# Optimization experiments

Hardware: AMD Instinct MI355X
Metric: run time of the kernel (lower is better)

## Reference

```python
import jax, jax.numpy as jnp
import numpy as np

B, D, N, H = 2, 512, 2048, 8
DK = D // H
EPS = 1e-5


def conv1x1(x, w, b):
    # kernel-size-1 Conv1d == channel-mixing GEMM: (o,i) x (b,i,n) -> (b,o,n)
    return jnp.einsum('oi,bin->bon', w, x) + b[None, :, None]


def setup_inputs() -> dict:
    key = jax.random.key(0)
    ks = jax.random.split(key, 20)
    s = 0.02
    return {
        'init_query': jax.random.normal(ks[0], (B, D, N), jnp.float32),
        'key_t': jax.random.normal(ks[1], (B, D, N), jnp.float32),
        'value': jax.random.normal(ks[2], (B, D, N), jnp.float32),
        'mask': jax.random.randint(ks[3], (B, 1, N, N), 0, 2, jnp.int32),
        'Wq': jax.random.normal(ks[4], (D, D), jnp.float32) * s,
        'bq': jax.random.normal(ks[5], (D,), jnp.float32) * s,
        'Wk': jax.random.normal(ks[6], (D, D), jnp.float32) * s,
        'bk': jax.random.normal(ks[7], (D,), jnp.float32) * s,
        'Wv': jax.random.normal(ks[8], (D, D), jnp.float32) * s,
        'bv': jax.random.normal(ks[9], (D,), jnp.float32) * s,
        'Wm': jax.random.normal(ks[10], (D, D), jnp.float32) * s,
        'bm': jax.random.normal(ks[11], (D,), jnp.float32) * s,
        'W1': jax.random.normal(ks[12], (2 * D, 2 * D), jnp.float32) * s,
        'b1': jax.random.normal(ks[13], (2 * D,), jnp.float32) * s,
        'gamma': jnp.ones((2 * D,), jnp.float32),
        'beta': jnp.zeros((2 * D,), jnp.float32),
        'rmean': jax.random.normal(ks[14], (2 * D,), jnp.float32) * s,
        'rvar': jnp.abs(jax.random.normal(ks[15], (2 * D,), jnp.float32)) * 0.1 + 0.5,
        'W2': jax.random.normal(ks[16], (D, 2 * D), jnp.float32) * s,
        'b2': jnp.zeros((D,), jnp.float32),  # nn.init.constant_(bias, 0.0)
    }


def reference(init_query, key_t, value, mask, Wq, bq, Wk, bk, Wv, bv, Wm, bm,
              W1, b1, gamma, beta, rmean, rvar, W2, b2):
    # projections, split channels into (d_k, n_heads) exactly like torch .view
    q = conv1x1(init_query, Wq, bq).reshape(B, DK, H, N)
    k = conv1x1(key_t, Wk, bk).reshape(B, DK, H, N)
    v = conv1x1(value, Wv, bv).reshape(B, DK, H, N)
    scores = jnp.einsum('bdhn,bdhm->bhnm', q, k) / jnp.sqrt(jnp.float32(DK))
    scores = jnp.where(mask == 0, jnp.float32(-1e9), scores)
    attn = jax.nn.softmax(scores, axis=-1)
    x = jnp.einsum('bhnm,bdhm->bdhn', attn, v).reshape(B, D, N)
    x = conv1x1(x, Wm, bm)
    x = jnp.concatenate([x, init_query], axis=1)  # (B, 2D, N)
    h = conv1x1(x, W1, b1)
    # BatchNorm1d (inference mode with running stats) + ReLU
    h = (h - rmean[None, :, None]) * (gamma / jnp.sqrt(rvar + EPS))[None, :, None] + beta[None, :, None]
    h = jax.nn.relu(h)
    return conv1x1(h, W2, b2)
```

## Files before the change

### kernel.cpp

```cpp
#include <hip/hip_runtime.h>

typedef unsigned short u16;
typedef unsigned int u32;
typedef unsigned long long u64;
typedef long long i64;
typedef __bf16 bf16x8 __attribute__((ext_vector_type(8)));
typedef u16 u16x8 __attribute__((ext_vector_type(8)));
typedef u32 u32x2 __attribute__((ext_vector_type(2)));
typedef float f32x4 __attribute__((ext_vector_type(4)));

#define DEV __device__ __forceinline__

constexpr int BB = 2, DD = 512, NN = 2048, HH = 8, DKc = 64, D2 = 1024;

constexpr float QSC = 0.125f * 1.44269504088896340736f;

constexpr i64 OFF_CAT = 0;
constexpr i64 OFF_XKT = 8388608;
constexpr i64 OFF_XVT = 12582912;
constexpr i64 OFF_QH  = 16777216;
constexpr i64 OFF_KH  = 20971520;
constexpr i64 OFF_VT  = 25165824;
constexpr i64 OFF_OT  = 29360128;
constexpr i64 OFF_HT  = 33554432;
constexpr i64 OFF_WQP = 41943040;
constexpr i64 OFF_WKP = 42467328;
constexpr i64 OFF_WVP = 42991616;
constexpr i64 OFF_WMP = 43515904;
constexpr i64 OFF_W1B = 44040192;
constexpr i64 OFF_W2B = 46137344;
constexpr i64 OFF_BQP = 47185920;
constexpr i64 OFF_BKP = 47187968;
constexpr i64 OFF_BVP = 47190016;
constexpr i64 OFF_BNA = 47192064;
constexpr i64 OFF_BNC = 47196160;
constexpr i64 OFF_MSK = 47200256;

DEV u16 f2bf(float f) {
  u32 u = __float_as_uint(f);
  u = u + 0x7FFFu + ((u >> 16) & 1u);
  return (u16)(u >> 16);
}

DEV u32 packbf(float lo, float hi) {
  return __builtin_amdgcn_perm(__float_as_uint(hi), __float_as_uint(lo), 0x07060302u);
}

DEV float fexp2(float x) {
#if __has_builtin(__builtin_amdgcn_exp2f)
  return __builtin_amdgcn_exp2f(x);
#else
  return exp2f(x);
#endif
}

DEV bf16x8 ldfrag(const u16* p) {
  bf16x8 v;
  __builtin_memcpy(&v, __builtin_assume_aligned(p, 16), 16);
  return v;
}

DEV bf16x8 ldfrag8(const u16* p) {
  bf16x8 v;
  __builtin_memcpy(&v, __builtin_assume_aligned(p, 8), 16);
  return v;
}

DEV bf16x8 ones8() {
  u16x8 u = {0x3F80, 0x3F80, 0x3F80, 0x3F80, 0x3F80, 0x3F80, 0x3F80, 0x3F80};
  bf16x8 v;
  __builtin_memcpy(&v, &u, 16);
  return v;
}

DEV void gload16(const void* g, void* lds) {
  __builtin_amdgcn_global_load_lds((__attribute__((address_space(1))) void*)g,
                                   (__attribute__((address_space(3))) void*)lds, 16, 0, 0);
}

DEV f32x4 mfma16(bf16x8 a, bf16x8 b, f32x4 c) {
  return __builtin_amdgcn_mfma_f32_16x16x32_bf16(a, b, c, 0, 0, 0);
}

__global__ __launch_bounds__(256) void prep_kernel(
    const float* __restrict__ Wq, const float* __restrict__ Wk, const float* __restrict__ Wv,
    const float* __restrict__ Wm, const float* __restrict__ W1, const float* __restrict__ W2,
    const float* __restrict__ bq, const float* __restrict__ bk, const float* __restrict__ bv,
    const float* __restrict__ b1, const float* __restrict__ gamma_, const float* __restrict__ beta_,
    const float* __restrict__ rmean, const float* __restrict__ rvar, const int* __restrict__ mask,
    u16* __restrict__ wqp, u16* __restrict__ wkp, u16* __restrict__ wvp, u16* __restrict__ wmp,
    u16* __restrict__ w1b, u16* __restrict__ w2b,
    float* __restrict__ bqp, float* __restrict__ bkp, float* __restrict__ bvp,
    float* __restrict__ bna, float* __restrict__ bnc, u32* __restrict__ mw) {
  const int blk = blockIdx.x, t = threadIdx.x;
  if (blk < 768) {
    const int which = blk >> 8, lb = blk & 255;
    const float* W = which == 0 ? Wq : (which == 1 ? Wk : Wv);
    u16* dst = which == 0 ? wqp : (which == 1 ? wkp : wvp);
    for (int e = lb * 256 + t; e < 262144; e += 65536) {
      int op = e >> 9, i = e & 511;
      int dk = op & 63, h = op >> 6;
      dst[e] = f2bf(W[(dk * 8 + h) * 512 + i]);
    }
  } else if (blk < 1024) {
    const int lb = blk - 768;
    for (int e = lb * 256 + t; e < 262144; e += 65536) {
      int o = e >> 9, c = e & 511;
      int dk = c & 63, h = c >> 6;
      wmp[e] = f2bf(Wm[o * 512 + dk * 8 + h]);
    }
  } else if (blk < 1536) {
    const int lb = blk - 1024;
    for (int e = lb * 256 + t; e < 1048576; e += 131072) w1b[e] = f2bf(W1[e]);
  } else if (blk < 1792) {
    const int lb = blk - 1536;
    for (int e = lb * 256 + t; e < 524288; e += 65536) w2b[e] = f2bf(W2[e]);
  } else if (blk == 1792) {
    for (int e = t; e < 512; e += 256) {
      int src = (e & 63) * 8 + (e >> 6);
      bqp[e] = bq[src]; bkp[e] = bk[src]; bvp[e] = bv[src];
    }
    for (int e = t; e < 1024; e += 256) {
      float a = gamma_[e] * rsqrtf(rvar[e] + 1e-5f);
      bna[e] = a;
      bnc[e] = (b1[e] - rmean[e]) * a + beta_[e];
    }
  } else {
    const int tid = (blk - 1793) * 256 + t;
    const i64 base = (i64)tid * 32;
    const int4* mp = (const int4*)(mask + base);
    u32 word = 0;
#pragma unroll
    for (int j = 0; j < 8; ++j) {
      int4 x = mp[j];
      u32 nib = (x.x != 0 ? 1u : 0u) | (x.y != 0 ? 2u : 0u) | (x.z != 0 ? 4u : 0u) |
                (x.w != 0 ? 8u : 0u);
      word |= nib << (j * 4);
    }
    mw[tid] = word;
  }
}

__global__ __launch_bounds__(256) void transpose_cvt(const float* __restrict__ iq,
                                                     const float* __restrict__ kt,
                                                     const float* __restrict__ vv,
                                                     u16* __restrict__ cat, u16* __restrict__ xkt,
                                                     u16* __restrict__ xvt) {
  __shared__ float tile[32][33];
  const int z = blockIdx.z, tensor = z >> 1, b = z & 1;
  const float* src = tensor == 0 ? iq : (tensor == 1 ? kt : vv);
  src += (i64)b * DD * NN;
  u16* dst; i64 ldd; int coff;
  if (tensor == 0)      { dst = cat + (i64)b * NN * D2; ldd = D2; coff = DD; }
  else if (tensor == 1) { dst = xkt + (i64)b * NN * DD; ldd = DD; coff = 0; }
  else                  { dst = xvt + (i64)b * NN * DD; ldd = DD; coff = 0; }
  const int x0 = blockIdx.x * 32, y0 = blockIdx.y * 32;
  const int col = threadIdx.x & 31, rg = threadIdx.x >> 5;
#pragma unroll
  for (int i = 0; i < 4; ++i) {
    int row = rg + i * 8;
    tile[row][col] = src[(i64)(y0 + row) * NN + x0 + col];
  }
  __syncthreads();
#pragma unroll
  for (int i = 0; i < 4; ++i) {
    int rr = rg + i * 8;
    dst[(i64)(x0 + rr) * ldd + coff + y0 + col] = f2bf(tile[col][rr]);
  }
}

template <int AM, int AN>
DEV void gemm_core(const u16* __restrict__ A, i64 lda, const u16* __restrict__ Bp, i64 ldb,
                   int K, u16* As, u16* Bs, f32x4 (&acc)[AM][AN]) {
  constexpr int BM = AM * 32, BN = AN * 32;
  const int t = threadIdx.x, w = t >> 6, l = t & 63, quad = l >> 4, l15 = l & 15;
  const int wm = (w >> 1) * AM * 16, wn = (w & 1) * AN * 16;
  for (int kk = 0; kk < K; kk += 64) {
    __syncthreads();
#pragma unroll
    for (int j = 0; j < BM / 32; ++j) {
      int ch = j * 256 + w * 64 + l, r = ch >> 3, c = ch & 7;
      gload16(A + (i64)r * lda + kk + ((c ^ (r & 7)) << 3), As + (j * 256 + w * 64) * 8);
    }
#pragma unroll
    for (int j = 0; j < BN / 32; ++j) {
      int ch = j * 256 + w * 64 + l, r = ch >> 3, c = ch & 7;
      gload16(Bp + (i64)r * ldb + kk + ((c ^ (r & 7)) << 3), Bs + (j * 256 + w * 64) * 8);
    }
    __syncthreads();
#pragma unroll
    for (int kc = 0; kc < 2; ++kc) {
      const int sw = ((kc * 4 + quad) ^ (l15 & 7)) << 3;
      bf16x8 af[AM], bfr[AN];
#pragma unroll
      for (int i = 0; i < AM; ++i) af[i] = ldfrag(&As[(wm + i * 16 + l15) * 64 + sw]);
#pragma unroll
      for (int j = 0; j < AN; ++j) bfr[j] = ldfrag(&Bs[(wn + j * 16 + l15) * 64 + sw]);
#pragma unroll
      for (int i = 0; i < AM; ++i)
#pragma unroll
        for (int j = 0; j < AN; ++j) acc[i][j] = mfma16(af[i], bfr[j], acc[i][j]);
    }
  }
}

__global__ __launch_bounds__(256) void qkv_gemm(const u16* __restrict__ cat,
                                                const u16* __restrict__ xkt,
                                                const u16* __restrict__ xvt,
                                                const u16* __restrict__ wqp,
                                                const u16* __restrict__ wkp,
                                                const u16* __restrict__ wvp,
                                                const float* __restrict__ bqp,
                                                const float* __restrict__ bkp,
                                                const float* __restrict__ bvp,
                                                u16* __restrict__ qh, u16* __restrict__ kh,
                                                u16* __restrict__ vt) {
  __shared__ __align__(16) u16 As[128 * 64];
  __shared__ __align__(16) u16 Bs[64 * 64];
  const int z = blockIdx.z, op = z >> 1, b = z & 1;
  const int t = threadIdx.x, w = t >> 6, l = t & 63, quad = l >> 4, l15 = l & 15;
  const int wm = (w >> 1) * 64, wn = (w & 1) * 32;
  int mx, ny;
  const u16 *A, *Bp;
  i64 lda, ldb;
  if (op < 2) {
    mx = blockIdx.x; ny = blockIdx.y;
    A = (op == 0 ? cat + DD : xkt);
    lda = (op == 0 ? D2 : DD);
    A += (i64)b * NN * lda + (i64)mx * 128 * lda;
    Bp = (op == 0 ? wqp : wkp) + (i64)ny * 64 * DD;
    ldb = DD;
  } else {
    int f = blockIdx.x * 8 + blockIdx.y;
    mx = f >> 5; ny = f & 31;
    A = wvp + (i64)mx * 128 * DD; lda = DD;
    Bp = xvt + (i64)b * NN * DD + (i64)ny * 64 * DD; ldb = DD;
  }
  f32x4 acc[4][2] = {};
  gemm_core<4, 2>(A, lda, Bp, ldb, DD, As, Bs, acc);

  const int rowBase = mx * 128 + wm + quad * 4;
  const int colBase = ny * 64 + wn + l15;
  if (op < 2) {
    const float* bias = (op == 0 ? bqp : bkp);
    const float sc = (op == 0 ? QSC : 1.f);
    u16* dst = (op == 0 ? qh : kh) + (i64)b * HH * NN * DKc;
#pragma unroll
    for (int j = 0; j < 2; ++j) {
      const int col = colBase + j * 16;
      const float cA = bias[col];
#pragma unroll
      for (int i = 0; i < 4; ++i)
#pragma unroll
        for (int r = 0; r < 4; ++r) {
          const int row = rowBase + i * 16 + r;
          dst[(i64)(col >> 6) * (NN * 64) + (i64)row * 64 + (col & 63)] =
              f2bf((acc[i][j][r] + cA) * sc);
        }
    }
  } else {
    u16* dst = vt + (i64)b * HH * DKc * NN;
#pragma unroll
    for (int j = 0; j < 2; ++j) {
      const int col = colBase + j * 16;
      const int colp = (col & ~63) | (((col & 15) << 2) | ((col >> 4) & 3));
#pragma unroll
      for (int i = 0; i < 4; ++i)
#pragma unroll
        for (int r = 0; r < 4; ++r) {
          const int row = rowBase + i * 16 + r;
          dst[(i64)row * NN + colp] = f2bf(acc[i][j][r] + bvp[row]);
        }
    }
  }
}

struct GArgs {
  const u16* A; i64 lda, sAb;
  const u16* B; i64 ldb, sBb;
  void* C; i64 ldc, sCb;
  const float* p1; const float* p2;
  int K;
};

template <int MODE, int AM, int AN>
__global__ __launch_bounds__(256) void gemm_bt(GArgs g) {
  __shared__ __align__(16) u16 As[AM * 32 * 64];
  __shared__ __align__(16) u16 Bs[AN * 32 * 64];
  const int t = threadIdx.x, w = t >> 6, l = t & 63, quad = l >> 4, l15 = l & 15;
  const int wm = (w >> 1) * AM * 16, wn = (w & 1) * AN * 16;
  const int bz = blockIdx.z;
  const u16* A = g.A + (i64)bz * g.sAb + (i64)blockIdx.x * (AM * 32) * g.lda;
  const u16* Bp = g.B + (i64)bz * g.sBb + (i64)blockIdx.y * (AN * 32) * g.ldb;
  f32x4 acc[AM][AN] = {};
  gemm_core<AM, AN>(A, g.lda, Bp, g.ldb, g.K, As, Bs, acc);

  const int rowBase = blockIdx.x * (AM * 32) + wm + quad * 4;
  const int colBase = blockIdx.y * (AN * 32) + wn + l15;
#pragma unroll
  for (int j = 0; j < AN; ++j) {
    const int col = colBase + j * 16;
    float cA = 0.f, cB = 0.f;
    if (MODE == 0) cA = g.p1[col];
    if (MODE == 3) { cA = g.p1[col]; cB = g.p2[col]; }
#pragma unroll
    for (int i = 0; i < AM; ++i) {
#pragma unroll
      for (int r = 0; r < 4; ++r) {
        const int row = rowBase + i * 16 + r;
        float v = acc[i][j][r];
        if (MODE == 0) {
          ((u16*)g.C + (i64)bz * g.sCb)[(i64)row * g.ldc + col] = f2bf(v + cA);
        } else if (MODE == 3) {
          float x = v * cA + cB;
          ((u16*)g.C + (i64)bz * g.sCb)[(i64)row * g.ldc + col] = f2bf(x > 0.f ? x : 0.f);
        } else {
          ((float*)g.C + (i64)bz * g.sCb)[(i64)row * g.ldc + col] = v + g.p1[row];
        }
      }
    }
  }
}

__global__ __launch_bounds__(256) void flash_attn(const u16* __restrict__ Qh,
                                                  const u16* __restrict__ Kh,
                                                  const u16* __restrict__ Vt,
                                                  const u64* __restrict__ MW,
                                                  u16* __restrict__ Ot) {
  __shared__ __align__(16) u16 Qs[64 * 64];
  __shared__ __align__(16) u16 Ks[64 * 64];
  __shared__ __align__(16) u16 Vs[64 * 64];
  __shared__ __align__(16) u16 Ps[4][16 * 68];
  const int t = threadIdx.x, w = t >> 6, l = t & 63, quad = l >> 4, l15 = l & 15;
  const int nt = blockIdx.x, h = blockIdx.y, b = blockIdx.z;
  const u16* Qb = Qh + ((i64)(b * HH + h) * NN + nt * 64) * 64;
  const u16* Kb = Kh + (i64)(b * HH + h) * NN * 64;
  const u16* Vb = Vt + (i64)(b * HH + h) * 64 * NN;
  const bf16x8 ONE = ones8();
#pragma unroll
  for (int j = 0; j < 2; ++j) {
    int ch = j * 256 + w * 64 + l, r = ch >> 3, c = ch & 7;
    gload16(Qb + r * 64 + ((c ^ (r & 7)) << 3), &Qs[(j * 256 + w * 64) * 8]);
  }
  __syncthreads();
  bf16x8 qf[2];
#pragma unroll
  for (int kc = 0; kc < 2; ++kc)
    qf[kc] = ldfrag(&Qs[(w * 16 + l15) * 64 + (((kc * 4 + quad) ^ (l15 & 7)) << 3)]);

  f32x4 oacc[4] = {};
  f32x4 lacc = {};
  for (int mt = 0; mt < NN / 64; ++mt) {
    __syncthreads();
#pragma unroll
    for (int j = 0; j < 2; ++j) {
      int ch = j * 256 + w * 64 + l, r = ch >> 3, c = ch & 7;
      gload16(Kb + (i64)mt * 4096 + r * 64 + ((c ^ (r & 7)) << 3), &Ks[(j * 256 + w * 64) * 8]);
      gload16(Vb + (i64)r * NN + mt * 64 + ((c ^ (r & 7)) << 3), &Vs[(j * 256 + w * 64) * 8]);
    }
    __syncthreads();
    f32x4 s[4];
#pragma unroll
    for (int ct = 0; ct < 4; ++ct) {
      const int sw = l15 & 7;
      bf16x8 k0 = ldfrag(&Ks[(ct * 16 + l15) * 64 + ((quad ^ sw) << 3)]);
      bf16x8 k1 = ldfrag(&Ks[(ct * 16 + l15) * 64 + (((4 + quad) ^ sw) << 3)]);
      f32x4 z = {};
      z = mfma16(qf[0], k0, z);
      z = mfma16(qf[1], k1, z);
      s[ct] = z;
    }
#pragma unroll
    for (int r = 0; r < 4; ++r) {
      int n = nt * 64 + w * 16 + quad * 4 + r;
      u64 sh = MW[(i64)(b * NN + n) * 32 + mt] >> l15;
      u32 m01 = ((u32)sh & 0x00010001u) * 0xFFFFu;
      u32 m23 = ((u32)(sh >> 32) & 0x00010001u) * 0xFFFFu;
      u32 w0 = packbf(fexp2(s[0][r]), fexp2(s[1][r])) & m01;
      u32 w1 = packbf(fexp2(s[2][r]), fexp2(s[3][r])) & m23;
      u32x2 pair = {w0, w1};
      __builtin_memcpy(__builtin_assume_aligned(&Ps[w][(quad * 4 + r) * 68 + l15 * 4], 8), &pair, 8);
    }
    asm volatile("" ::: "memory");
    bf16x8 pf0 = ldfrag8(&Ps[w][l15 * 68 + quad * 8]);
    bf16x8 pf1 = ldfrag8(&Ps[w][l15 * 68 + 32 + quad * 8]);
    lacc = mfma16(pf0, ONE, lacc);
    lacc = mfma16(pf1, ONE, lacc);
#pragma unroll
    for (int dt = 0; dt < 4; ++dt) {
      const int sw = l15 & 7;
      bf16x8 v0 = ldfrag(&Vs[(dt * 16 + l15) * 64 + ((quad ^ sw) << 3)]);
      bf16x8 v1 = ldfrag(&Vs[(dt * 16 + l15) * 64 + (((4 + quad) ^ sw) << 3)]);
      oacc[dt] = mfma16(pf0, v0, oacc[dt]);
      oacc[dt] = mfma16(pf1, v1, oacc[dt]);
    }
  }
  float inv[4];
#pragma unroll
  for (int r = 0; r < 4; ++r) inv[r] = __builtin_amdgcn_rcpf(lacc[r]);
#pragma unroll
  for (int dt = 0; dt < 4; ++dt)
#pragma unroll
    for (int r = 0; r < 4; ++r) {
      int n = nt * 64 + w * 16 + quad * 4 + r;
      Ot[((i64)b * NN + n) * DD + h * DKc + dt * 16 + l15] = f2bf(oacc[dt][r] * inv[r]);
    }
}

extern "C" void kernel_launch(void* const* d_in, const int* in_sizes, int n_in,
                              void* d_out, int out_size, void* d_ws, size_t ws_size,
                              hipStream_t stream) {
  (void)in_sizes; (void)n_in; (void)out_size; (void)ws_size;
  const float* iq    = (const float*)d_in[0];
  const float* kt    = (const float*)d_in[1];
  const float* vv    = (const float*)d_in[2];
  const int*   mask  = (const int*)d_in[3];
  const float* Wq    = (const float*)d_in[4];
  const float* bq    = (const float*)d_in[5];
  const float* Wk    = (const float*)d_in[6];
  const float* bk    = (const float*)d_in[7];
  const float* Wv    = (const float*)d_in[8];
  const float* bv    = (const float*)d_in[9];
  const float* Wm    = (const float*)d_in[10];
  const float* bm    = (const float*)d_in[11];
  const float* W1    = (const float*)d_in[12];
  const float* b1    = (const float*)d_in[13];
  const float* gamma_= (const float*)d_in[14];
  const float* beta_ = (const float*)d_in[15];
  const float* rmean = (const float*)d_in[16];
  const float* rvar  = (const float*)d_in[17];
  const float* W2    = (const float*)d_in[18];
  const float* b2    = (const float*)d_in[19];

  char* ws = (char*)d_ws;
  u16* cat = (u16*)(ws + OFF_CAT);
  u16* xkt = (u16*)(ws + OFF_XKT);
  u16* xvt = (u16*)(ws + OFF_XVT);
  u16* qh  = (u16*)(ws + OFF_QH);
  u16* kh  = (u16*)(ws + OFF_KH);
  u16* vt  = (u16*)(ws + OFF_VT);
  u16* ot  = (u16*)(ws + OFF_OT);
  u16* ht  = (u16*)(ws + OFF_HT);
  u16* wqp = (u16*)(ws + OFF_WQP);
  u16* wkp = (u16*)(ws + OFF_WKP);
  u16* wvp = (u16*)(ws + OFF_WVP);
  u16* wmp = (u16*)(ws + OFF_WMP);
  u16* w1b = (u16*)(ws + OFF_W1B);
  u16* w2b = (u16*)(ws + OFF_W2B);
  float* bqp = (float*)(ws + OFF_BQP);
  float* bkp = (float*)(ws + OFF_BKP);
  float* bvp = (float*)(ws + OFF_BVP);
  float* bna = (float*)(ws + OFF_BNA);
  float* bnc = (float*)(ws + OFF_BNC);
  u32* mw = (u32*)(ws + OFF_MSK);

  prep_kernel<<<2817, 256, 0, stream>>>(Wq, Wk, Wv, Wm, W1, W2, bq, bk, bv, b1, gamma_, beta_,
                                        rmean, rvar, mask, wqp, wkp, wvp, wmp, w1b, w2b,
                                        bqp, bkp, bvp, bna, bnc, mw);
  transpose_cvt<<<dim3(64, 16, 6), 256, 0, stream>>>(iq, kt, vv, cat, xkt, xvt);

  qkv_gemm<<<dim3(16, 8, 6), 256, 0, stream>>>(cat, xkt, xvt, wqp, wkp, wvp, bqp, bkp, bvp,
                                               qh, kh, vt);

  flash_attn<<<dim3(32, 8, 2), 256, 0, stream>>>(qh, kh, vt, (const u64*)mw, ot);

  GArgs ma{ot, DD, (i64)NN * DD, wmp, DD, 0, cat, D2, (i64)NN * D2, bm, nullptr, DD};
  gemm_bt<0, 2, 2><<<dim3(32, 8, 2), 256, 0, stream>>>(ma);
  GArgs wa{cat, D2, (i64)NN * D2, w1b, D2, 0, ht, D2, (i64)NN * D2, bna, bnc, D2};
  gemm_bt<3, 4, 2><<<dim3(16, 16, 2), 256, 0, stream>>>(wa);
  GArgs w2a{w2b, D2, 0, ht, D2, (i64)NN * D2, d_out, NN, (i64)DD * NN, b2, nullptr, D2};
  gemm_bt<4, 2, 2><<<dim3(8, 32, 2), 256, 0, stream>>>(w2a);
}
```

Measured before the change: 233.5 us.

## Fold merge projection into W1 and split attention KV range with combine

```diff
diff --git a/kernel.cpp b/kernel.cpp
--- a/kernel.cpp
+++ b/kernel.cpp
@@ -18,29 +18,32 @@
 constexpr i64 OFF_CAT = 0;
 constexpr i64 OFF_XKT = 8388608;
 constexpr i64 OFF_XVT = 12582912;
+constexpr i64 OFF_HT  = 8388608;
 constexpr i64 OFF_QH  = 16777216;
 constexpr i64 OFF_KH  = 20971520;
 constexpr i64 OFF_VT  = 25165824;
-constexpr i64 OFF_OT  = 29360128;
-constexpr i64 OFF_HT  = 33554432;
-constexpr i64 OFF_WQP = 41943040;
-constexpr i64 OFF_WKP = 42467328;
-constexpr i64 OFF_WVP = 42991616;
-constexpr i64 OFF_WMP = 43515904;
-constexpr i64 OFF_W1B = 44040192;
-constexpr i64 OFF_W2B = 46137344;
-constexpr i64 OFF_BQP = 47185920;
-constexpr i64 OFF_BKP = 47187968;
-constexpr i64 OFF_BVP = 47190016;
-constexpr i64 OFF_BNA = 47192064;
-constexpr i64 OFF_BNC = 47196160;
-constexpr i64 OFF_MSK = 47200256;
+constexpr i64 OFF_WQP = 29360128;
+constexpr i64 OFF_WKP = 29884416;
+constexpr i64 OFF_WVP = 30408704;
+constexpr i64 OFF_WMT = 30932992;
+constexpr i64 OFF_W1A = 31457280;
+constexpr i64 OFF_W1C = 32505856;
+constexpr i64 OFF_W2B = 34603008;
+constexpr i64 OFF_BQP = 35651584;
+constexpr i64 OFF_BKP = 35653632;
+constexpr i64 OFF_BVP = 35655680;
+constexpr i64 OFF_BNA = 35657728;
+constexpr i64 OFF_BNC = 35661824;
+constexpr i64 OFF_LP  = 35665920;
+constexpr i64 OFF_MSK = 35928064;
 
 DEV u16 f2bf(float f) {
   u32 u = __float_as_uint(f);
   u = u + 0x7FFFu + ((u >> 16) & 1u);
   return (u16)(u >> 16);
 }
+
+DEV float bf2f(u16 u) { return __uint_as_float(((u32)u) << 16); }
 
 DEV u32 packbf(float lo, float hi) {
   return __builtin_amdgcn_perm(__float_as_uint(hi), __float_as_uint(lo), 0x07060302u);
@@ -86,10 +89,11 @@
     const float* __restrict__ Wq, const float* __restrict__ Wk, const float* __restrict__ Wv,
     const float* __restrict__ Wm, const float* __restrict__ W1, const float* __restrict__ W2,
     const float* __restrict__ bq, const float* __restrict__ bk, const float* __restrict__ bv,
-    const float* __restrict__ b1, const float* __restrict__ gamma_, const float* __restrict__ beta_,
-    const float* __restrict__ rmean, const float* __restrict__ rvar, const int* __restrict__ mask,
-    u16* __restrict__ wqp, u16* __restrict__ wkp, u16* __restrict__ wvp, u16* __restrict__ wmp,
-    u16* __restrict__ w1b, u16* __restrict__ w2b,
+    const float* __restrict__ bm, const float* __restrict__ b1, const float* __restrict__ gamma_,
+    const float* __restrict__ beta_, const float* __restrict__ rmean,
+    const float* __restrict__ rvar, const int* __restrict__ mask,
+    u16* __restrict__ wqp, u16* __restrict__ wkp, u16* __restrict__ wvp, u16* __restrict__ wmt,
+    u16* __restrict__ w1a, u16* __restrict__ w1c, u16* __restrict__ w2b,
     float* __restrict__ bqp, float* __restrict__ bkp, float* __restrict__ bvp,
     float* __restrict__ bna, float* __restrict__ bnc, u32* __restrict__ mw) {
   const int blk = blockIdx.x, t = threadIdx.x;
@@ -105,28 +109,53 @@
   } else if (blk < 1024) {
     const int lb = blk - 768;
     for (int e = lb * 256 + t; e < 262144; e += 65536) {
-      int o = e >> 9, c = e & 511;
-      int dk = c & 63, h = c >> 6;
-      wmp[e] = f2bf(Wm[o * 512 + dk * 8 + h]);
+      int cp = e >> 9, o = e & 511;
+      int dk = cp & 63, h = cp >> 6;
+      wmt[e] = f2bf(Wm[o * 512 + dk * 8 + h]);
+    }
+  } else if (blk < 1280) {
+    const int lb = blk - 1024;
+    for (int e = lb * 256 + t; e < 524288; e += 65536) {
+      int row = e >> 9, o = e & 511;
+      w1a[e] = f2bf(W1[(i64)row * 1024 + o]);
     }
   } else if (blk < 1536) {
-    const int lb = blk - 1024;
-    for (int e = lb * 256 + t; e < 1048576; e += 131072) w1b[e] = f2bf(W1[e]);
+    const int lb = blk - 1280;
+    for (int e = lb * 256 + t; e < 524288; e += 65536) {
+      int row = e >> 9, j = e & 511;
+      w1c[(i64)row * 1024 + 512 + j] = f2bf(W1[(i64)row * 1024 + 512 + j]);
+    }
   } else if (blk < 1792) {
     const int lb = blk - 1536;
     for (int e = lb * 256 + t; e < 524288; e += 65536) w2b[e] = f2bf(W2[e]);
-  } else if (blk == 1792) {
+  } else if (blk < 1808) {
+    __shared__ float sm[4][64];
+    const int base = (blk - 1792) * 64;
+    const int el = t & 63, oq = t >> 6;
+    const float* wrow = W1 + (i64)(base + el) * 1024 + oq * 128;
+    const float* bmq = bm + oq * 128;
+    float s = 0.f;
+#pragma unroll 8
+    for (int j = 0; j < 128; j += 4) {
+      float4 x = *(const float4*)(wrow + j);
+      float4 y = *(const float4*)(bmq + j);
+      s += x.x * y.x + x.y * y.y + x.z * y.z + x.w * y.w;
+    }
+    sm[oq][el] = s;
+    __syncthreads();
+    if (t < 64) {
+      int e = base + t;
+      float a = gamma_[e] * rsqrtf(rvar[e] + 1e-5f);
+      bna[e] = a;
+      bnc[e] = (b1[e] - rmean[e]) * a + beta_[e] + a * (sm[0][t] + sm[1][t] + sm[2][t] + sm[3][t]);
+    }
+  } else if (blk == 1808) {
     for (int e = t; e < 512; e += 256) {
       int src = (e & 63) * 8 + (e >> 6);
       bqp[e] = bq[src]; bkp[e] = bk[src]; bvp[e] = bv[src];
     }
-    for (int e = t; e < 1024; e += 256) {
-      float a = gamma_[e] * rsqrtf(rvar[e] + 1e-5f);
-      bna[e] = a;
-      bnc[e] = (b1[e] - rmean[e]) * a + beta_[e];
-    }
   } else {
-    const int tid = (blk - 1793) * 256 + t;
+    const int tid = (blk - 1809) * 256 + t;
     const i64 base = (i64)tid * 32;
     const int4* mp = (const int4*)(mask + base);
     u32 word = 0;
@@ -162,10 +191,14 @@
     tile[row][col] = src[(i64)(y0 + row) * NN + x0 + col];
   }
   __syncthreads();
-#pragma unroll
-  for (int i = 0; i < 4; ++i) {
-    int rr = rg + i * 8;
-    dst[(i64)(x0 + rr) * ldd + coff + y0 + col] = f2bf(tile[col][rr]);
+  const int dp = threadIdx.x & 15, rbase = threadIdx.x >> 4;
+  u32* dst32 = (u32*)dst;
+  const i64 ldw = ldd >> 1;
+  const int cw = (coff + y0) >> 1;
+#pragma unroll
+  for (int i = 0; i < 2; ++i) {
+    int rr = rbase + i * 16;
+    dst32[(i64)(x0 + rr) * ldw + cw + dp] = packbf(tile[2 * dp][rr], tile[2 * dp + 1][rr]);
   }
 }
 
@@ -301,7 +334,6 @@
   for (int j = 0; j < AN; ++j) {
     const int col = colBase + j * 16;
     float cA = 0.f, cB = 0.f;
-    if (MODE == 0) cA = g.p1[col];
     if (MODE == 3) { cA = g.p1[col]; cB = g.p2[col]; }
 #pragma unroll
     for (int i = 0; i < AM; ++i) {
@@ -309,13 +341,13 @@
       for (int r = 0; r < 4; ++r) {
         const int row = rowBase + i * 16 + r;
         float v = acc[i][j][r];
-        if (MODE == 0) {
-          ((u16*)g.C + (i64)bz * g.sCb)[(i64)row * g.ldc + col] = f2bf(v + cA);
-        } else if (MODE == 3) {
+        if (MODE == 3) {
           float x = v * cA + cB;
           ((u16*)g.C + (i64)bz * g.sCb)[(i64)row * g.ldc + col] = f2bf(x > 0.f ? x : 0.f);
+        } else if (MODE == 4) {
+          ((float*)g.C + (i64)bz * g.sCb)[(i64)row * g.ldc + col] = v + g.p1[row];
         } else {
-          ((float*)g.C + (i64)bz * g.sCb)[(i64)row * g.ldc + col] = v + g.p1[row];
+          ((u16*)g.C + (i64)bz * g.sCb)[(i64)row * g.ldc + col] = f2bf(v);
         }
       }
     }
@@ -326,13 +358,14 @@
                                                   const u16* __restrict__ Kh,
                                                   const u16* __restrict__ Vt,
                                                   const u64* __restrict__ MW,
-                                                  u16* __restrict__ Ot) {
+                                                  u16* __restrict__ Opart,
+                                                  float* __restrict__ Lp) {
   __shared__ __align__(16) u16 Qs[64 * 64];
   __shared__ __align__(16) u16 Ks[64 * 64];
   __shared__ __align__(16) u16 Vs[64 * 64];
   __shared__ __align__(16) u16 Ps[4][16 * 68];
   const int t = threadIdx.x, w = t >> 6, l = t & 63, quad = l >> 4, l15 = l & 15;
-  const int nt = blockIdx.x, h = blockIdx.y, b = blockIdx.z;
+  const int nt = blockIdx.x, h = blockIdx.y, b = blockIdx.z >> 1, sp = blockIdx.z & 1;
   const u16* Qb = Qh + ((i64)(b * HH + h) * NN + nt * 64) * 64;
   const u16* Kb = Kh + (i64)(b * HH + h) * NN * 64;
   const u16* Vb = Vt + (i64)(b * HH + h) * 64 * NN;
@@ -350,7 +383,8 @@
 
   f32x4 oacc[4] = {};
   f32x4 lacc = {};
-  for (int mt = 0; mt < NN / 64; ++mt) {
+  const int mt0 = sp * 16, mt1 = mt0 + 16;
+  for (int mt = mt0; mt < mt1; ++mt) {
     __syncthreads();
 #pragma unroll
     for (int j = 0; j < 2; ++j) {
@@ -395,16 +429,42 @@
       oacc[dt] = mfma16(pf1, v1, oacc[dt]);
     }
   }
-  float inv[4];
-#pragma unroll
-  for (int r = 0; r < 4; ++r) inv[r] = __builtin_amdgcn_rcpf(lacc[r]);
+  u16* Op = Opart + (i64)sp * BB * NN * DD;
 #pragma unroll
   for (int dt = 0; dt < 4; ++dt)
 #pragma unroll
     for (int r = 0; r < 4; ++r) {
       int n = nt * 64 + w * 16 + quad * 4 + r;
-      Ot[((i64)b * NN + n) * DD + h * DKc + dt * 16 + l15] = f2bf(oacc[dt][r] * inv[r]);
-    }
+      Op[((i64)b * NN + n) * DD + h * DKc + dt * 16 + l15] = f2bf(oacc[dt][r]);
+    }
+  if (l15 == 0) {
+#pragma unroll
+    for (int r = 0; r < 4; ++r) {
+      int n = nt * 64 + w * 16 + quad * 4 + r;
+      Lp[((i64)(sp * BB + b) * HH + h) * NN + n] = lacc[r];
+    }
+  }
+}
+
+__global__ __launch_bounds__(256) void combine(const u16* __restrict__ Opart,
+                                               const float* __restrict__ Lp,
+                                               u16* __restrict__ cat) {
+  const int tid = blockIdx.x * 256 + threadIdx.x;
+  const int b = tid >> 18, rem = tid & 262143;
+  const int n = rem >> 7, cq = rem & 127;
+  const int c0 = cq << 2, h = c0 >> 6;
+  const u16* p0 = Opart + ((i64)b * NN + n) * DD + c0;
+  const u16* p1 = p0 + (i64)BB * NN * DD;
+  u16 a0[4], a1[4];
+  __builtin_memcpy(a0, __builtin_assume_aligned(p0, 8), 8);
+  __builtin_memcpy(a1, __builtin_assume_aligned(p1, 8), 8);
+  float l0 = Lp[((i64)b * HH + h) * NN + n];
+  float l1 = Lp[((i64)(BB + b) * HH + h) * NN + n];
+  float rl = __builtin_amdgcn_rcpf(l0 + l1);
+  u16 o[4];
+#pragma unroll
+  for (int j = 0; j < 4; ++j) o[j] = f2bf((bf2f(a0[j]) + bf2f(a1[j])) * rl);
+  __builtin_memcpy(__builtin_assume_aligned(&cat[((i64)b * NN + n) * D2 + c0], 8), o, 8);
 }
 
 extern "C" void kernel_launch(void* const* d_in, const int* in_sizes, int n_in,
@@ -436,37 +496,41 @@
   u16* cat = (u16*)(ws + OFF_CAT);
   u16* xkt = (u16*)(ws + OFF_XKT);
   u16* xvt = (u16*)(ws + OFF_XVT);
+  u16* ht  = (u16*)(ws + OFF_HT);
   u16* qh  = (u16*)(ws + OFF_QH);
   u16* kh  = (u16*)(ws + OFF_KH);
   u16* vt  = (u16*)(ws + OFF_VT);
-  u16* ot  = (u16*)(ws + OFF_OT);
-  u16* ht  = (u16*)(ws + OFF_HT);
   u16* wqp = (u16*)(ws + OFF_WQP);
   u16* wkp = (u16*)(ws + OFF_WKP);
   u16* wvp = (u16*)(ws + OFF_WVP);
-  u16* wmp = (u16*)(ws + OFF_WMP);
-  u16* w1b = (u16*)(ws + OFF_W1B);
+  u16* wmt = (u16*)(ws + OFF_WMT);
+  u16* w1a = (u16*)(ws + OFF_W1A);
+  u16* w1c = (u16*)(ws + OFF_W1C);
   u16* w2b = (u16*)(ws + OFF_W2B);
   float* bqp = (float*)(ws + OFF_BQP);
   float* bkp = (float*)(ws + OFF_BKP);
   float* bvp = (float*)(ws + OFF_BVP);
   float* bna = (float*)(ws + OFF_BNA);
   float* bnc = (float*)(ws + OFF_BNC);
+  float* lp  = (float*)(ws + OFF_LP);
   u32* mw = (u32*)(ws + OFF_MSK);
-
-  prep_kernel<<<2817, 256, 0, stream>>>(Wq, Wk, Wv, Wm, W1, W2, bq, bk, bv, b1, gamma_, beta_,
-                                        rmean, rvar, mask, wqp, wkp, wvp, wmp, w1b, w2b,
-                                        bqp, bkp, bvp, bna, bnc, mw);
+  u16* opart = (u16*)(ws + OFF_XKT);
+
+  prep_kernel<<<2833, 256, 0, stream>>>(Wq, Wk, Wv, Wm, W1, W2, bq, bk, bv, bm, b1, gamma_,
+                                        beta_, rmean, rvar, mask, wqp, wkp, wvp, wmt, w1a, w1c,
+                                        w2b, bqp, bkp, bvp, bna, bnc, mw);
   transpose_cvt<<<dim3(64, 16, 6), 256, 0, stream>>>(iq, kt, vv, cat, xkt, xvt);
+
+  GArgs ca{w1a, DD, 0, wmt, DD, 0, w1c, D2, 0, nullptr, nullptr, DD};
+  gemm_bt<5, 4, 2><<<dim3(8, 8, 1), 256, 0, stream>>>(ca);
 
   qkv_gemm<<<dim3(16, 8, 6), 256, 0, stream>>>(cat, xkt, xvt, wqp, wkp, wvp, bqp, bkp, bvp,
                                                qh, kh, vt);
 
-  flash_attn<<<dim3(32, 8, 2), 256, 0, stream>>>(qh, kh, vt, (const u64*)mw, ot);
-
-  GArgs ma{ot, DD, (i64)NN * DD, wmp, DD, 0, cat, D2, (i64)NN * D2, bm, nullptr, DD};
-  gemm_bt<0, 2, 2><<<dim3(32, 8, 2), 256, 0, stream>>>(ma);
-  GArgs wa{cat, D2, (i64)NN * D2, w1b, D2, 0, ht, D2, (i64)NN * D2, bna, bnc, D2};
+  flash_attn<<<dim3(32, 8, 4), 256, 0, stream>>>(qh, kh, vt, (const u64*)mw, opart, lp);
+  combine<<<2048, 256, 0, stream>>>(opart, lp, cat);
+
+  GArgs wa{cat, D2, (i64)NN * D2, w1c, D2, 0, ht, D2, (i64)NN * D2, bna, bnc, D2};
   gemm_bt<3, 4, 2><<<dim3(16, 16, 2), 256, 0, stream>>>(wa);
   GArgs w2a{w2b, D2, 0, ht, D2, (i64)NN * D2, d_out, NN, (i64)DD * NN, b2, nullptr, D2};
   gemm_bt<4, 2, 2><<<dim3(8, 32, 2), 256, 0, stream>>>(w2a);
```

Result: no change. 237.9 us (+1.9%).
